# Optimization experiments

Hardware: AMD Instinct MI355X
Metric: run time of the kernel (lower is better)

Reference implementation:

```python
import jax, jax.numpy as jnp
import numpy as np


def setup_inputs() -> dict:
    key = jax.random.key(0)
    k1, k2, k3, k4, k5 = jax.random.split(key, 5)
    N, M, K = 200000, 50, 4
    T = 1000.0
    ti = jnp.sort(jax.random.uniform(k1, (N,), dtype=jnp.float32) * T)
    mi = jax.random.randint(k2, (N,), 0, M, dtype=jnp.int64)
    mu_at_events = jax.random.uniform(k3, (N,), dtype=jnp.float32) * 0.5 + 0.05
    alpha = jax.random.uniform(k4, (K, M, M), dtype=jnp.float32) * 0.1
    gamma = jax.random.uniform(k5, (K,), dtype=jnp.float32) * 2.0 + 0.5
    return {"ti": ti, "mi": mi, "mu_at_events": mu_at_events, "alpha": alpha, "gamma": gamma}


def _hawkes_logsum(ti, mi, mu_at_events, alpha, gamma):
    # ti: [N] sorted event times; mi: [N] event types in [0, M)
    # alpha: [K, M, M]; gamma: [K]; mu_at_events: [N]
    N = ti.shape[0]
    M = alpha.shape[1]
    # inter-event gaps; dt[0] = 0 so the first event has zero excitation state
    dt = jnp.concatenate([jnp.zeros((1,), ti.dtype), ti[1:] - ti[:-1]])  # [N]
    a = jnp.exp(-gamma[None, :] * dt[:, None])  # [N, K] decay factors
    # one-hot of the PREVIOUS event's type (row 0 is all-zero, matching e_mi)
    prev_onehot = jnp.zeros((N, M), ti.dtype).at[jnp.arange(1, N), mi[:-1]].set(1.0)
    b = a[:, None, :] * prev_onehot[:, :, None]  # [N, M, K]

    # linear recurrence S_i = a_i * S_{i-1} + b_i via associative scan
    # combine((a1,b1),(a2,b2)) = (a1*a2, a2*b1 + b2)
    def combine(x, y):
        a1, b1 = x
        a2, b2 = y
        return (a1 * a2, a2[:, None, :] * b1 + b2)

    _, S = jax.lax.associative_scan(combine, (a, b))  # S: [N, M, K]
    # S[i, m, k] = sum_{j < i, m_j = m} exp(-gamma_k (t_i - t_j))
    alpha_at = alpha[:, mi, :]  # [K, N, M] rows of alpha for each event's type
    lam = mu_at_events + jnp.einsum('knm,nmk,k->n', alpha_at, S, gamma)  # [N]
    return jnp.sum(jnp.log(lam))


def reference(ti, mi, mu_at_events, alpha, gamma):
    return _hawkes_logsum(ti, mi, mu_at_events, alpha, gamma)
```

## Files before the change

kernel.cpp:

```cpp
#include <hip/hip_runtime.h>
#include <hip/hip_bf16.h>

#define CHUNK 256
#define MM 50
#define KK 4
#define STATE (MM*KK)
#define ASTRIDE 51
#define SUP 32
#define NSMAX 26
#define NSUB 8
#define SUBSZ 32

__device__ __forceinline__ unsigned short f2bf(float x) {
  unsigned u = __float_as_uint(x);
  u += 0x7fffu + ((u >> 16) & 1u);
  return (unsigned short)(u >> 16);
}

__global__ __launch_bounds__(256) void phase1(
    const float* __restrict__ ti, const int* __restrict__ mi,
    const float* __restrict__ gamma, float* __restrict__ chunkB,
    float* __restrict__ out0, int N, int G) {
  int g = blockIdx.x, tid = threadIdx.x;
  if (g == 0 && tid == 0) out0[0] = 0.f;
  int l = g * CHUNK;
  int r = min(N, l + CHUNK);
  __shared__ float Bs[STATE];
  __shared__ float g4[KK];
  if (tid < STATE) Bs[tid] = 0.f;
  if (tid < KK) g4[tid] = gamma[tid];
  __syncthreads();
  float t_end = ti[r - 1];
  int j0 = (g == 0) ? 0 : (l - 1);
  int j = j0 + tid;
  if (j <= r - 2) {
    int m = mi[j];
    float dt = t_end - ti[j];
    #pragma unroll
    for (int k = 0; k < KK; ++k)
      atomicAdd(&Bs[m * KK + k], __expf(-g4[k] * dt));
  }
  __syncthreads();
  if (tid < STATE) chunkB[(size_t)g * STATE + tid] = Bs[tid];
}

__global__ __launch_bounds__(256) void phase2a(
    const float* __restrict__ ti, const float* __restrict__ gamma,
    const float* __restrict__ chunkB, float* __restrict__ localpref,
    float* __restrict__ superB, int N, int G) {
  int s = blockIdx.x, tid = threadIdx.x;
  int g0 = s * SUP;
  int gN = min(G, g0 + SUP) - g0;
  __shared__ float te[SUP + 1];
  if (tid <= SUP) {
    int gg = g0 + tid;
    te[tid] = (gg == 0) ? ti[0] : ti[min(N, gg * CHUNK) - 1];
  }
  __syncthreads();
  if (tid >= STATE) return;
  float gk = gamma[tid & 3];
  float B[SUP];
  #pragma unroll
  for (int u = 0; u < SUP; ++u)
    B[u] = (u < gN) ? chunkB[(size_t)(g0 + u) * STATE + tid] : 0.f;
  float S = 0.f;
  #pragma unroll
  for (int u = 0; u < SUP; ++u) {
    if (u < gN) {
      localpref[(size_t)(g0 + u) * STATE + tid] = S;
      if (u == 0) {
        S = B[0];
      } else {
        float a = __expf(-gk * (te[u + 1] - te[u]));
        S = a * S + B[u];
      }
    }
  }
  superB[(size_t)s * STATE + tid] = S;
}

__global__ __launch_bounds__(256) void phase2b(
    const float* __restrict__ ti, const float* __restrict__ gamma,
    const float* __restrict__ superB, float* __restrict__ superpref,
    int N, int nS) {
  int tid = threadIdx.x;
  __shared__ float tlast[NSMAX];
  if (tid < NSMAX)
    tlast[tid] = ti[min(SUP * (tid + 1) * CHUNK, N) - 1];
  __syncthreads();
  if (tid >= STATE) return;
  float gk = gamma[tid & 3];
  float B[NSMAX];
  #pragma unroll
  for (int s = 0; s < NSMAX; ++s)
    B[s] = (s < nS) ? superB[(size_t)s * STATE + tid] : 0.f;
  float S = 0.f;
  superpref[tid] = 0.f;
  #pragma unroll
  for (int s = 0; s < NSMAX; ++s) {
    if (s < nS) {
      if (s == 0) S = B[0];
      else {
        float a = __expf(-gk * (tlast[s] - tlast[s - 1]));
        S = a * S + B[s];
      }
      if (s + 1 < nS) superpref[(size_t)(s + 1) * STATE + tid] = S;
    }
  }
}

__global__ __launch_bounds__(256) void phase3(
    const float* __restrict__ ti, const int* __restrict__ mi,
    const float* __restrict__ mu, const float* __restrict__ alpha,
    const float* __restrict__ gamma, const float* __restrict__ localpref,
    const float* __restrict__ superpref, float* __restrict__ out, int N, int G) {
  int g = blockIdx.x, tid = threadIdx.x;
  int l = g * CHUNK;
  int r = min(N, l + CHUNK);
  int cnt = r - l;
  int sup = g / SUP;

  __shared__ unsigned P0[MM * ASTRIDE];
  __shared__ unsigned P1[MM * ASTRIDE];
  __shared__ __align__(16) float4 Fj[CHUNK];
  __shared__ int   cj[CHUNK];
  __shared__ __align__(16) float Q[NSUB][STATE];
  __shared__ float red[256];

  float gk0 = gamma[0], gk1 = gamma[1], gk2 = gamma[2], gk3 = gamma[3];

  for (int i = tid; i < NSUB * STATE; i += 256) ((float*)Q)[i] = 0.f;

  for (int e = tid; e < MM * MM; e += 256) {
    int c = e / MM, cp = e - c * MM;
    float a0 = gk0 * alpha[e];
    float a1 = gk1 * alpha[2500 + e];
    float a2 = gk2 * alpha[5000 + e];
    float a3 = gk3 * alpha[7500 + e];
    P0[c * ASTRIDE + cp] = (unsigned)f2bf(a0) | ((unsigned)f2bf(a1) << 16);
    P1[c * ASTRIDE + cp] = (unsigned)f2bf(a2) | ((unsigned)f2bf(a3) << 16);
  }

  int j = l - 1 + tid;
  float t_ref = ti[(g == 0) ? 0 : (l - 1)];
  float4 myF = make_float4(0.f, 0.f, 0.f, 0.f);
  int myc = 0;
  bool valid = (j >= 0) && (j <= r - 2);
  if (valid) {
    myc = mi[j];
    float tj = ti[j] - t_ref;
    myF = make_float4(__expf(gk0 * tj), __expf(gk1 * tj),
                      __expf(gk2 * tj), __expf(gk3 * tj));
  }
  cj[tid] = myc;
  Fj[tid] = myF;
  __syncthreads();

  if (valid) {
    float* q = &Q[tid >> 5][myc * KK];
    atomicAdd(q + 0, myF.x); atomicAdd(q + 1, myF.y);
    atomicAdd(q + 2, myF.z); atomicAdd(q + 3, myF.w);
  }
  __syncthreads();

  if (tid < STATE) {
    float gk = gamma[tid & 3];
    float t_lo = (sup > 0) ? ti[(size_t)sup * SUP * CHUNK - 1] : ti[0];
    float D = __expf(-gk * (t_ref - t_lo));
    float run = localpref[(size_t)g * STATE + tid]
              + D * superpref[(size_t)sup * STATE + tid];
    #pragma unroll
    for (int q = 0; q < NSUB; ++q) {
      float t = Q[q][tid];
      Q[q][tid] = run;
      run += t;
    }
  }
  __syncthreads();

  float local = 0.f;
  if (tid < cnt) {
    int n = l + tid;
    int c_n = mi[n];
    int rowb = c_n * ASTRIDE;
    const float4* wb = (const float4*)&Q[tid >> 5][0];
    float4 acc = make_float4(0.f, 0.f, 0.f, 0.f);
    #pragma unroll 2
    for (int m = 0; m < MM; ++m) {
      unsigned p0 = P0[rowb + m];
      unsigned p1 = P1[rowb + m];
      float4 w = wb[m];
      acc.x += __uint_as_float(p0 << 16)         * w.x;
      acc.y += __uint_as_float(p0 & 0xffff0000u) * w.y;
      acc.z += __uint_as_float(p1 << 16)         * w.z;
      acc.w += __uint_as_float(p1 & 0xffff0000u) * w.w;
    }
    #pragma unroll 4
    for (int s = (tid & ~(SUBSZ - 1)); s <= tid; ++s) {
      unsigned p0 = P0[rowb + cj[s]];
      unsigned p1 = P1[rowb + cj[s]];
      float4 f = Fj[s];
      acc.x += __uint_as_float(p0 << 16)         * f.x;
      acc.y += __uint_as_float(p0 & 0xffff0000u) * f.y;
      acc.z += __uint_as_float(p1 << 16)         * f.z;
      acc.w += __uint_as_float(p1 & 0xffff0000u) * f.w;
    }
    float tn = ti[n] - t_ref;
    float lam = mu[n]
              + __expf(-gk0 * tn) * acc.x + __expf(-gk1 * tn) * acc.y
              + __expf(-gk2 * tn) * acc.z + __expf(-gk3 * tn) * acc.w;
    local = __logf(lam);
  }
  red[tid] = local;
  __syncthreads();
  for (int off = 128; off > 0; off >>= 1) {
    if (tid < off) red[tid] += red[tid + off];
    __syncthreads();
  }
  if (tid == 0) atomicAdd(out, red[0]);
}

extern "C" void kernel_launch(void* const* d_in, const int* in_sizes, int n_in,
                              void* d_out, int out_size, void* d_ws, size_t ws_size,
                              hipStream_t stream) {
  const float* ti    = (const float*)d_in[0];
  const int*   mi    = (const int*)d_in[1];
  const float* mu    = (const float*)d_in[2];
  const float* alpha = (const float*)d_in[3];
  const float* gamma = (const float*)d_in[4];
  float* out = (float*)d_out;
  int N = in_sizes[0];
  int G = (N + CHUNK - 1) / CHUNK;
  int nS = (G + SUP - 1) / SUP;
  float* chunkB    = (float*)d_ws;
  float* localpref = chunkB + (size_t)G * STATE;
  float* superB    = localpref + (size_t)G * STATE;
  float* superpref = superB + (size_t)NSMAX * STATE;

  phase1<<<G, 256, 0, stream>>>(ti, mi, gamma, chunkB, out, N, G);
  phase2a<<<nS, 256, 0, stream>>>(ti, gamma, chunkB, localpref, superB, N, G);
  phase2b<<<1, 256, 0, stream>>>(ti, gamma, superB, superpref, N, nS);
  phase3<<<G, 256, 0, stream>>>(ti, mi, mu, alpha, gamma, localpref, superpref, out, N, G);
}
```

Before: 103.5 us.

## Replace serial scan kernels with atomic super-chunk sums and direct prefix recomputation

```diff
diff --git a/kernel.cpp b/kernel.cpp
--- a/kernel.cpp
+++ b/kernel.cpp
@@ -20,7 +20,7 @@
 __global__ __launch_bounds__(256) void phase1(
     const float* __restrict__ ti, const int* __restrict__ mi,
     const float* __restrict__ gamma, float* __restrict__ chunkB,
-    float* __restrict__ out0, int N, int G) {
+    float* __restrict__ superB, float* __restrict__ out0, int N, int G) {
   int g = blockIdx.x, tid = threadIdx.x;
   if (g == 0 && tid == 0) out0[0] = 0.f;
   int l = g * CHUNK;
@@ -41,84 +41,27 @@
       atomicAdd(&Bs[m * KK + k], __expf(-g4[k] * dt));
   }
   __syncthreads();
-  if (tid < STATE) chunkB[(size_t)g * STATE + tid] = Bs[tid];
-}
-
-__global__ __launch_bounds__(256) void phase2a(
-    const float* __restrict__ ti, const float* __restrict__ gamma,
-    const float* __restrict__ chunkB, float* __restrict__ localpref,
-    float* __restrict__ superB, int N, int G) {
-  int s = blockIdx.x, tid = threadIdx.x;
-  int g0 = s * SUP;
-  int gN = min(G, g0 + SUP) - g0;
-  __shared__ float te[SUP + 1];
-  if (tid <= SUP) {
-    int gg = g0 + tid;
-    te[tid] = (gg == 0) ? ti[0] : ti[min(N, gg * CHUNK) - 1];
-  }
-  __syncthreads();
-  if (tid >= STATE) return;
-  float gk = gamma[tid & 3];
-  float B[SUP];
-  #pragma unroll
-  for (int u = 0; u < SUP; ++u)
-    B[u] = (u < gN) ? chunkB[(size_t)(g0 + u) * STATE + tid] : 0.f;
-  float S = 0.f;
-  #pragma unroll
-  for (int u = 0; u < SUP; ++u) {
-    if (u < gN) {
-      localpref[(size_t)(g0 + u) * STATE + tid] = S;
-      if (u == 0) {
-        S = B[0];
-      } else {
-        float a = __expf(-gk * (te[u + 1] - te[u]));
-        S = a * S + B[u];
-      }
-    }
-  }
-  superB[(size_t)s * STATE + tid] = S;
-}
-
-__global__ __launch_bounds__(256) void phase2b(
-    const float* __restrict__ ti, const float* __restrict__ gamma,
-    const float* __restrict__ superB, float* __restrict__ superpref,
-    int N, int nS) {
-  int tid = threadIdx.x;
-  __shared__ float tlast[NSMAX];
-  if (tid < NSMAX)
-    tlast[tid] = ti[min(SUP * (tid + 1) * CHUNK, N) - 1];
-  __syncthreads();
-  if (tid >= STATE) return;
-  float gk = gamma[tid & 3];
-  float B[NSMAX];
-  #pragma unroll
-  for (int s = 0; s < NSMAX; ++s)
-    B[s] = (s < nS) ? superB[(size_t)s * STATE + tid] : 0.f;
-  float S = 0.f;
-  superpref[tid] = 0.f;
-  #pragma unroll
-  for (int s = 0; s < NSMAX; ++s) {
-    if (s < nS) {
-      if (s == 0) S = B[0];
-      else {
-        float a = __expf(-gk * (tlast[s] - tlast[s - 1]));
-        S = a * S + B[s];
-      }
-      if (s + 1 < nS) superpref[(size_t)(s + 1) * STATE + tid] = S;
-    }
+  if (tid < STATE) {
+    float v = Bs[tid];
+    chunkB[(size_t)g * STATE + tid] = v;
+    int sup = g / SUP;
+    float gk = g4[tid & 3];
+    float Tsup = ti[min(N, (sup + 1) * SUP * CHUNK) - 1];
+    atomicAdd(&superB[(size_t)sup * STATE + tid], __expf(-gk * (Tsup - t_end)) * v);
   }
 }
 
 __global__ __launch_bounds__(256) void phase3(
     const float* __restrict__ ti, const int* __restrict__ mi,
     const float* __restrict__ mu, const float* __restrict__ alpha,
-    const float* __restrict__ gamma, const float* __restrict__ localpref,
-    const float* __restrict__ superpref, float* __restrict__ out, int N, int G) {
+    const float* __restrict__ gamma, const float* __restrict__ chunkB,
+    const float* __restrict__ superB, float* __restrict__ out, int N, int G) {
   int g = blockIdx.x, tid = threadIdx.x;
   int l = g * CHUNK;
   int r = min(N, l + CHUNK);
   int cnt = r - l;
   int sup = g / SUP;
+  int g0 = sup * SUP;
 
   __shared__ unsigned P0[MM * ASTRIDE];
   __shared__ unsigned P1[MM * ASTRIDE];
@@ -126,6 +69,8 @@
   __shared__ int   cj[CHUNK];
   __shared__ __align__(16) float Q[NSUB][STATE];
   __shared__ float red[256];
+  __shared__ float teL[SUP];
+  __shared__ float tlast[NSMAX];
 
   float gk0 = gamma[0], gk1 = gamma[1], gk2 = gamma[2], gk3 = gamma[3];
 
@@ -139,6 +84,14 @@
     float a3 = gk3 * alpha[7500 + e];
     P0[c * ASTRIDE + cp] = (unsigned)f2bf(a0) | ((unsigned)f2bf(a1) << 16);
     P1[c * ASTRIDE + cp] = (unsigned)f2bf(a2) | ((unsigned)f2bf(a3) << 16);
+  }
+
+  if (tid < SUP) {
+    int c = g0 + tid;
+    if (c < G) teL[tid] = ti[min(N, (c + 1) * CHUNK) - 1];
+  } else if (tid >= 64 && tid < 64 + NSMAX) {
+    int s = tid - 64;
+    if (s < sup) tlast[s] = ti[min(N, (s + 1) * SUP * CHUNK) - 1];
   }
 
   int j = l - 1 + tid;
@@ -161,14 +114,22 @@
     atomicAdd(q + 0, myF.x); atomicAdd(q + 1, myF.y);
     atomicAdd(q + 2, myF.z); atomicAdd(q + 3, myF.w);
   }
-  __syncthreads();
-
+
+  float S = 0.f;
   if (tid < STATE) {
     float gk = gamma[tid & 3];
-    float t_lo = (sup > 0) ? ti[(size_t)sup * SUP * CHUNK - 1] : ti[0];
-    float D = __expf(-gk * (t_ref - t_lo));
-    float run = localpref[(size_t)g * STATE + tid]
-              + D * superpref[(size_t)sup * STATE + tid];
+    int nloc = g - g0;
+    #pragma unroll 4
+    for (int u = 0; u < nloc; ++u)
+      S += __expf(-gk * (t_ref - teL[u])) * chunkB[(size_t)(g0 + u) * STATE + tid];
+    #pragma unroll 4
+    for (int s = 0; s < sup; ++s)
+      S += __expf(-gk * (t_ref - tlast[s])) * superB[(size_t)s * STATE + tid];
+  }
+  __syncthreads();
+
+  if (tid < STATE) {
+    float run = S;
     #pragma unroll
     for (int q = 0; q < NSUB; ++q) {
       float t = Q[q][tid];
@@ -185,7 +146,7 @@
     int rowb = c_n * ASTRIDE;
     const float4* wb = (const float4*)&Q[tid >> 5][0];
     float4 acc = make_float4(0.f, 0.f, 0.f, 0.f);
-    #pragma unroll 2
+    #pragma unroll 5
     for (int m = 0; m < MM; ++m) {
       unsigned p0 = P0[rowb + m];
       unsigned p1 = P1[rowb + m];
@@ -232,13 +193,10 @@
   int N = in_sizes[0];
   int G = (N + CHUNK - 1) / CHUNK;
   int nS = (G + SUP - 1) / SUP;
-  float* chunkB    = (float*)d_ws;
-  float* localpref = chunkB + (size_t)G * STATE;
-  float* superB    = localpref + (size_t)G * STATE;
-  float* superpref = superB + (size_t)NSMAX * STATE;
-
-  phase1<<<G, 256, 0, stream>>>(ti, mi, gamma, chunkB, out, N, G);
-  phase2a<<<nS, 256, 0, stream>>>(ti, gamma, chunkB, localpref, superB, N, G);
-  phase2b<<<1, 256, 0, stream>>>(ti, gamma, superB, superpref, N, nS);
-  phase3<<<G, 256, 0, stream>>>(ti, mi, mu, alpha, gamma, localpref, superpref, out, N, G);
-}
+  float* chunkB = (float*)d_ws;
+  float* superB = chunkB + (size_t)G * STATE;
+
+  hipMemsetAsync(superB, 0, (size_t)nS * STATE * sizeof(float), stream);
+  phase1<<<G, 256, 0, stream>>>(ti, mi, gamma, chunkB, superB, out, N, G);
+  phase3<<<G, 256, 0, stream>>>(ti, mi, mu, alpha, gamma, chunkB, superB, out, N, G);
+}
```

After: 95.42 us. 1.08x faster.
